# Kernel tuning notes

Hardware: AMD Instinct MI355X
Metric: run time of the kernel (lower is better)

## Reference

```python
import jax, jax.numpy as jnp
import numpy as np

HEADS = 16
DIM = 1024


def setup_inputs() -> dict:
    key = jax.random.key(0)
    ks = jax.random.split(key, 9)
    B, N, D = 2, 2048, DIM
    s = 1.0 / np.sqrt(D)
    x = jax.random.normal(ks[0], (B, N, D), dtype=jnp.float32)
    Wq = jax.random.normal(ks[1], (D, D), dtype=jnp.float32) * s
    Wk = jax.random.normal(ks[2], (D, D), dtype=jnp.float32) * s
    Wv = jax.random.normal(ks[3], (D, D), dtype=jnp.float32) * s
    Wo = jax.random.normal(ks[4], (D, D), dtype=jnp.float32) * s
    bq = jax.random.normal(ks[5], (D,), dtype=jnp.float32) * 0.01
    bk = jax.random.normal(ks[6], (D,), dtype=jnp.float32) * 0.01
    bv = jax.random.normal(ks[7], (D,), dtype=jnp.float32) * 0.01
    bo = jax.random.normal(ks[8], (D,), dtype=jnp.float32) * 0.01
    return {"x": x, "Wq": Wq, "bq": bq, "Wk": Wk, "bk": bk,
            "Wv": Wv, "bv": bv, "Wo": Wo, "bo": bo}


def reference(x, Wq, bq, Wk, bk, Wv, bv, Wo, bo):
    B, N, D = x.shape
    H = HEADS
    hd = D // H
    scale = hd ** (-0.5)
    # projections; split heads -> [B, H, N, hd]
    q = (x @ Wq + bq).reshape(B, N, H, hd).transpose(0, 2, 1, 3)
    k = (x @ Wk + bk).reshape(B, N, H, hd).transpose(0, 2, 1, 3)
    v = (x @ Wv + bv).reshape(B, N, H, hd).transpose(0, 2, 1, 3)
    # full [B, H, N, N] scores (faithful to naive torch implementation)
    attn = jnp.einsum('bhqd,bhkd->bhqk', q, k) * scale
    attn = jax.nn.softmax(attn, axis=-1)
    # dropout is identity in eval mode
    out = jnp.einsum('bhqk,bhkd->bhqd', attn, v)
    out = out.transpose(0, 2, 1, 3).reshape(B, N, D)
    return out @ Wo + bo
```

## Files before the change

kernel.cpp:

```cpp
#include <hip/hip_runtime.h>

#define HEADS 16
#define HD 64
#define SEQ 2048
#define DMODEL 1024
#define BATCH 2
#define MTOT (BATCH*SEQ)
#define KVB 64
#define NKH 16

typedef unsigned short u16;
typedef __bf16 bf16;
typedef bf16 bf16x8 __attribute__((ext_vector_type(8)));
typedef float f32x4 __attribute__((ext_vector_type(4)));
typedef float f32x16 __attribute__((ext_vector_type(16)));
typedef unsigned short u16x8 __attribute__((ext_vector_type(8)));
typedef unsigned short u16x4 __attribute__((ext_vector_type(4)));

static __device__ __forceinline__ u16 f2bf(float f) {
  bf16 b = (bf16)f;
  return __builtin_bit_cast(u16, b);
}

static __device__ __forceinline__ void async16(u16* lds_base, const u16* g) {
  __builtin_amdgcn_global_load_lds(
      (const __attribute__((address_space(1))) unsigned int*)g,
      (__attribute__((address_space(3))) unsigned int*)lds_base,
      16, 0, 0);
}

__global__ __launch_bounds__(256) void k_cvt(const float* __restrict__ in,
                                             u16* __restrict__ out, int n8) {
  int i = blockIdx.x * blockDim.x + threadIdx.x;
  if (i >= n8) return;
  const float4* p = (const float4*)(in + (size_t)i * 8);
  float4 a = p[0], b = p[1];
  u16x8 r;
  r[0] = f2bf(a.x); r[1] = f2bf(a.y); r[2] = f2bf(a.z); r[3] = f2bf(a.w);
  r[4] = f2bf(b.x); r[5] = f2bf(b.y); r[6] = f2bf(b.z); r[7] = f2bf(b.w);
  *(u16x8*)(out + (size_t)i * 8) = r;
}

__global__ __launch_bounds__(256) void k_cvtT(const float* __restrict__ W0, const float* __restrict__ W1,
                                              const float* __restrict__ W2, const float* __restrict__ W3,
                                              u16* __restrict__ T0, u16* __restrict__ T1,
                                              u16* __restrict__ T2, u16* __restrict__ T3) {
  const float* W = blockIdx.z == 0 ? W0 : blockIdx.z == 1 ? W1 : blockIdx.z == 2 ? W2 : W3;
  u16*         T = blockIdx.z == 0 ? T0 : blockIdx.z == 1 ? T1 : blockIdx.z == 2 ? T2 : T3;
  __shared__ u16 tile[64 * 68];
  int t = threadIdx.x;
  int kb = blockIdx.y * 64, nb = blockIdx.x * 64;
#pragma unroll
  for (int i = 0; i < 4; ++i) {
    int c = t * 4 + i;
    int row = c >> 4;
    int c4 = c & 15;
    float4 v = *(const float4*)&W[(size_t)(kb + row) * DMODEL + nb + c4 * 4];
    tile[row * 68 + c4 * 4 + 0] = f2bf(v.x);
    tile[row * 68 + c4 * 4 + 1] = f2bf(v.y);
    tile[row * 68 + c4 * 4 + 2] = f2bf(v.z);
    tile[row * 68 + c4 * 4 + 3] = f2bf(v.w);
  }
  __syncthreads();
#pragma unroll
  for (int i = 0; i < 2; ++i) {
    int c = t * 2 + i;
    int n = c >> 3;
    int k8 = c & 7;
    u16x8 v;
#pragma unroll
    for (int e = 0; e < 8; ++e) v[e] = tile[(k8 * 8 + e) * 68 + n];
    *(u16x8*)&T[(size_t)(nb + n) * DMODEL + kb + k8 * 8] = v;
  }
}

template <int MODE>
__global__ __launch_bounds__(256) void k_gemm(
    const u16* __restrict__ A,
    const u16* __restrict__ BT0, const u16* __restrict__ BT1, const u16* __restrict__ BT2,
    const float* __restrict__ b0, const float* __restrict__ b1, const float* __restrict__ b2,
    void* __restrict__ O0, void* __restrict__ O1, void* __restrict__ O2,
    int M, int N, int K) {
  const u16* BT = blockIdx.z == 0 ? BT0 : blockIdx.z == 1 ? BT1 : BT2;
  const float* bias = blockIdx.z == 0 ? b0 : blockIdx.z == 1 ? b1 : b2;
  void* Out = blockIdx.z == 0 ? O0 : blockIdx.z == 1 ? O1 : O2;

  __shared__ u16 Ads[2][128 * 32];
  __shared__ u16 Bds[2][128 * 32];
  int tid = threadIdx.x, wid = tid >> 6, lane = tid & 63;
  int r = lane & 15, g = lane >> 4;
  int wm = wid >> 1, wn = wid & 1;
  int m0 = blockIdx.y * 128, n0 = blockIdx.x * 128;

  f32x4 acc[4][4];
  f32x4 zero4 = {0.f, 0.f, 0.f, 0.f};
#pragma unroll
  for (int mt = 0; mt < 4; ++mt)
#pragma unroll
    for (int nt = 0; nt < 4; ++nt) acc[mt][nt] = zero4;

  int srow = lane >> 2;
  int scb = lane & 3;

  auto STAGE = [&](int b, int k0) {
#pragma unroll
    for (int tt = 0; tt < 2; ++tt) {
      int inst = wid * 2 + tt;
      int row = inst * 16 + srow;
      async16(&Ads[b][inst * 512], &A[(size_t)(m0 + row) * K + k0 + scb * 8]);
      async16(&Bds[b][inst * 512], &BT[(size_t)(n0 + row) * K + k0 + scb * 8]);
    }
  };

  auto BODY = [&](int buf, int k0) {
    if (k0 + 32 < K) STAGE(buf ^ 1, k0 + 32);
    bf16x8 af[4], bfv[4];
#pragma unroll
    for (int mt = 0; mt < 4; ++mt)
      af[mt] = *(const bf16x8*)&Ads[buf][(wm * 64 + mt * 16 + r) * 32 + g * 8];
#pragma unroll
    for (int nt = 0; nt < 4; ++nt)
      bfv[nt] = *(const bf16x8*)&Bds[buf][(wn * 64 + nt * 16 + r) * 32 + g * 8];
#pragma unroll
    for (int mt = 0; mt < 4; ++mt)
#pragma unroll
      for (int nt = 0; nt < 4; ++nt)
        acc[mt][nt] = __builtin_amdgcn_mfma_f32_16x16x32_bf16(af[mt], bfv[nt], acc[mt][nt], 0, 0, 0);
    asm volatile("s_waitcnt vmcnt(0)" ::: "memory");
    __builtin_amdgcn_sched_barrier(0);
    __builtin_amdgcn_s_barrier();
    __builtin_amdgcn_sched_barrier(0);
  };

  STAGE(0, 0);
  asm volatile("s_waitcnt vmcnt(0)" ::: "memory");
  __builtin_amdgcn_sched_barrier(0);
  __builtin_amdgcn_s_barrier();
  __builtin_amdgcn_sched_barrier(0);

  for (int k0 = 0; k0 < K; k0 += 64) {
    BODY(0, k0);
    BODY(1, k0 + 32);
  }

  const float qs = 0.18033688011112042f;
#pragma unroll
  for (int nt = 0; nt < 4; ++nt) {
    int col = n0 + wn * 64 + nt * 16 + r;
    float bv = bias[col];
#pragma unroll
    for (int mt = 0; mt < 4; ++mt) {
      int rowb = m0 + wm * 64 + mt * 16 + g * 4;
      if (MODE == 0) {
        int b = rowb >> 11;
        int h = col >> 6, d = col & (HD - 1);
        if (blockIdx.z == 2) {
          int n = rowb & (SEQ - 1);
          int np = (n & ~12) | ((n & 4) << 1) | ((n & 8) >> 1);
          u16x4 pk;
#pragma unroll
          for (int j = 0; j < 4; ++j) pk[j] = f2bf(acc[mt][nt][j] + bv);
          *(u16x4*)&((u16*)Out)[((size_t)((b * HEADS + h) * HD + d)) * SEQ + np] = pk;
        } else {
          float sc = (blockIdx.z == 0) ? qs : 1.0f;
#pragma unroll
          for (int j = 0; j < 4; ++j) {
            int row = rowb + j;
            int n = row & (SEQ - 1);
            ((u16*)Out)[((size_t)(b * HEADS + h) * SEQ + n) * HD + d] = f2bf((acc[mt][nt][j] + bv) * sc);
          }
        }
      } else {
#pragma unroll
        for (int j = 0; j < 4; ++j)
          ((float*)Out)[(size_t)(rowb + j) * N + col] = acc[mt][nt][j] + bv;
      }
    }
  }
}

__global__ __launch_bounds__(512, 2) void k_attn(const u16* __restrict__ Q,
                                                 const u16* __restrict__ Kg,
                                                 const u16* __restrict__ Vt,
                                                 u16* __restrict__ Oa) {
  __shared__ u16 lds[2][2][2][KVB * 64];

  int tid = threadIdx.x, wid = tid >> 6, lane = tid & 63;
  int l31 = lane & 31, hi = lane >> 5;
  int h = wid >> 2, s = wid & 3;

  int fid = blockIdx.y * gridDim.x + blockIdx.x;
  int swz = (fid & 7) * 32 + (fid >> 3);
  int qt = swz & 7;
  int bh = swz >> 3;

  const size_t kbase = (size_t)bh * SEQ * HD;
  const size_t vbase = (size_t)bh * HD * SEQ;
  int qA = qt * 256 + s * 64;

  bf16x8 qfA[4], qfB[4];
#pragma unroll
  for (int db = 0; db < 4; ++db) {
    qfA[db] = *(const bf16x8*)&Q[kbase + (size_t)(qA + l31) * HD + db * 16 + hi * 8];
    qfB[db] = *(const bf16x8*)&Q[kbase + (size_t)(qA + 32 + l31) * HD + db * 16 + hi * 8];
  }

  int swz7 = l31 & 7;
  int coff[4];
#pragma unroll
  for (int i = 0; i < 4; ++i) coff[i] = ((2 * i + hi) ^ swz7) * 8;

  f32x16 zero16 = {0.f,0.f,0.f,0.f,0.f,0.f,0.f,0.f,0.f,0.f,0.f,0.f,0.f,0.f,0.f,0.f};
  f32x16 oa0A = zero16, oa1A = zero16, lA = zero16;
  f32x16 oa0B = zero16, oa1B = zero16, lB = zero16;

  u16x8 onesb;
#pragma unroll
  for (int e = 0; e < 8; ++e) onesb[e] = 0x3F80;
  bf16x8 ones = __builtin_bit_cast(bf16x8, onesb);

  auto STAGE = [&](int b, int kc) {
    int kof = (h * NKH + kc) * KVB;
#pragma unroll
    for (int i = 0; i < 2; ++i) {
      int inst = s * 2 + i;
      int rr = inst * 8 + (lane >> 3);
      int ch = (lane & 7) ^ (rr & 7);
      async16(&lds[b][h][0][inst * 512], &Kg[kbase + (size_t)(kof + rr) * HD + ch * 8]);
      async16(&lds[b][h][1][inst * 512], &Vt[vbase + (size_t)rr * SEQ + kof + ch * 8]);
    }
  };

  auto BODY = [&](int buf, int kc) {
    if (kc + 1 < NKH) STAGE(buf ^ 1, kc + 1);

    const u16* Kb = &lds[buf][h][0][0];
    const u16* Vb = &lds[buf][h][1][0];

    f32x16 s0A = zero16, s1A = zero16, s0B = zero16, s1B = zero16;
#pragma unroll
    for (int db = 0; db < 4; ++db) {
      bf16x8 kf0 = *(const bf16x8*)&Kb[l31 * 64 + coff[db]];
      bf16x8 kf1 = *(const bf16x8*)&Kb[2048 + l31 * 64 + coff[db]];
      s0A = __builtin_amdgcn_mfma_f32_32x32x16_bf16(kf0, qfA[db], s0A, 0, 0, 0);
      s1A = __builtin_amdgcn_mfma_f32_32x32x16_bf16(kf1, qfA[db], s1A, 0, 0, 0);
      s0B = __builtin_amdgcn_mfma_f32_32x32x16_bf16(kf0, qfB[db], s0B, 0, 0, 0);
      s1B = __builtin_amdgcn_mfma_f32_32x32x16_bf16(kf1, qfB[db], s1B, 0, 0, 0);
    }

#pragma unroll
    for (int t = 0; t < 4; ++t) {
      u16x8 pkA, pkB;
#pragma unroll
      for (int e = 0; e < 8; ++e) {
        float svA = (t & 2) ? ((t & 1) ? s1A[8 + e] : s1A[e])
                            : ((t & 1) ? s0A[8 + e] : s0A[e]);
        float svB = (t & 2) ? ((t & 1) ? s1B[8 + e] : s1B[e])
                            : ((t & 1) ? s0B[8 + e] : s0B[e]);
        pkA[e] = f2bf(__builtin_amdgcn_exp2f(svA));
        pkB[e] = f2bf(__builtin_amdgcn_exp2f(svB));
      }
      bf16x8 paA = __builtin_bit_cast(bf16x8, pkA);
      bf16x8 paB = __builtin_bit_cast(bf16x8, pkB);

      bf16x8 vf0 = *(const bf16x8*)&Vb[l31 * 64 + coff[t]];
      bf16x8 vf1 = *(const bf16x8*)&Vb[2048 + l31 * 64 + coff[t]];
      lA   = __builtin_amdgcn_mfma_f32_32x32x16_bf16(paA, ones, lA, 0, 0, 0);
      oa0A = __builtin_amdgcn_mfma_f32_32x32x16_bf16(paA, vf0, oa0A, 0, 0, 0);
      oa1A = __builtin_amdgcn_mfma_f32_32x32x16_bf16(paA, vf1, oa1A, 0, 0, 0);
      lB   = __builtin_amdgcn_mfma_f32_32x32x16_bf16(paB, ones, lB, 0, 0, 0);
      oa0B = __builtin_amdgcn_mfma_f32_32x32x16_bf16(paB, vf0, oa0B, 0, 0, 0);
      oa1B = __builtin_amdgcn_mfma_f32_32x32x16_bf16(paB, vf1, oa1B, 0, 0, 0);
    }

    asm volatile("s_waitcnt vmcnt(0)" ::: "memory");
    __builtin_amdgcn_sched_barrier(0);
    __builtin_amdgcn_s_barrier();
    __builtin_amdgcn_sched_barrier(0);
  };

  STAGE(0, 0);
  asm volatile("s_waitcnt vmcnt(0)" ::: "memory");
  __builtin_amdgcn_sched_barrier(0);
  __builtin_amdgcn_s_barrier();
  __builtin_amdgcn_sched_barrier(0);

  for (int kc = 0; kc < NKH; kc += 2) {
    BODY(0, kc);
    BODY(1, kc + 1);
  }

  float* cf = (float*)&lds[0][0][0][0];
  int b = bh >> 4, hh = bh & 15;

  if (h == 1) {
#pragma unroll
    for (int r = 0; r < 16; ++r) {
      cf[s * 3072 + r * 64 + lane]        = oa0A[r];
      cf[s * 3072 + 1024 + r * 64 + lane] = oa1A[r];
      cf[s * 3072 + 2048 + r * 64 + lane] = lA[r];
    }
  }
  __syncthreads();
  if (h == 0) {
#pragma unroll
    for (int reg = 0; reg < 16; ++reg) {
      float o0 = oa0A[reg] + cf[s * 3072 + reg * 64 + lane];
      float o1 = oa1A[reg] + cf[s * 3072 + 1024 + reg * 64 + lane];
      float lv = lA[reg]   + cf[s * 3072 + 2048 + reg * 64 + lane];
      float inv = 1.0f / lv;
      int q = qA + (reg & 3) + 8 * (reg >> 2) + 4 * hi;
      size_t rowoff = ((size_t)(b * SEQ + q)) * DMODEL + hh * HD;
      Oa[rowoff + l31]      = f2bf(o0 * inv);
      Oa[rowoff + 32 + l31] = f2bf(o1 * inv);
    }
  }
  __syncthreads();
  if (h == 1) {
#pragma unroll
    for (int r = 0; r < 16; ++r) {
      cf[s * 3072 + r * 64 + lane]        = oa0B[r];
      cf[s * 3072 + 1024 + r * 64 + lane] = oa1B[r];
      cf[s * 3072 + 2048 + r * 64 + lane] = lB[r];
    }
  }
  __syncthreads();
  if (h == 0) {
#pragma unroll
    for (int reg = 0; reg < 16; ++reg) {
      float o0 = oa0B[reg] + cf[s * 3072 + reg * 64 + lane];
      float o1 = oa1B[reg] + cf[s * 3072 + 1024 + reg * 64 + lane];
      float lv = lB[reg]   + cf[s * 3072 + 2048 + reg * 64 + lane];
      float inv = 1.0f / lv;
      int q = qA + 32 + (reg & 3) + 8 * (reg >> 2) + 4 * hi;
      size_t rowoff = ((size_t)(b * SEQ + q)) * DMODEL + hh * HD;
      Oa[rowoff + l31]      = f2bf(o0 * inv);
      Oa[rowoff + 32 + l31] = f2bf(o1 * inv);
    }
  }
}

extern "C" void kernel_launch(void* const* d_in, const int* in_sizes, int n_in,
                              void* d_out, int out_size, void* d_ws, size_t ws_size,
                              hipStream_t stream) {
  const float* x  = (const float*)d_in[0];
  const float* Wq = (const float*)d_in[1];
  const float* bq = (const float*)d_in[2];
  const float* Wk = (const float*)d_in[3];
  const float* bk = (const float*)d_in[4];
  const float* Wv = (const float*)d_in[5];
  const float* bv = (const float*)d_in[6];
  const float* Wo = (const float*)d_in[7];
  const float* bo = (const float*)d_in[8];

  char* ws = (char*)d_ws;
  const size_t MB = 1024 * 1024;
  u16* xb    = (u16*)(ws);
  u16* wqT   = (u16*)(ws + 8 * MB);
  u16* wkT   = (u16*)(ws + 10 * MB);
  u16* wvT   = (u16*)(ws + 12 * MB);
  u16* woT   = (u16*)(ws + 14 * MB);
  u16* qbuf  = (u16*)(ws + 16 * MB);
  u16* kbuf  = (u16*)(ws + 24 * MB);
  u16* vbufT = (u16*)(ws + 32 * MB);
  u16* abuf  = (u16*)(ws + 40 * MB);

  k_cvt<<<2048, 256, 0, stream>>>(x, xb, (MTOT * DMODEL) / 8);
  k_cvtT<<<dim3(16, 16, 4), 256, 0, stream>>>(Wq, Wk, Wv, Wo, wqT, wkT, wvT, woT);
  k_gemm<0><<<dim3(DMODEL / 128, MTOT / 128, 3), 256, 0, stream>>>(
      xb, wqT, wkT, wvT, bq, bk, bv, qbuf, kbuf, vbufT, MTOT, DMODEL, DMODEL);
  k_attn<<<dim3(SEQ / 256, BATCH * HEADS), 512, 0, stream>>>(qbuf, kbuf, vbufT, abuf);
  k_gemm<1><<<dim3(DMODEL / 128, MTOT / 128, 1), 256, 0, stream>>>(
      abuf, woT, woT, woT, bo, bo, bo, d_out, d_out, d_out, MTOT, DMODEL, DMODEL);
}
```

Baseline: 111.2 us.

## Split-K output projection GEMM across two wave groups with LDS reduction

Replaces the templated output-projection GEMM with a dedicated 512-thread kernel. Two halves of the block each process half of K for the same 128x128 tile, and their partial accumulators are reduced through LDS before the bias is added and the result written. The output projection launches only 256 tiles of 256 threads, so this is meant to put more waves on each CU and hide latency, with a swizzled tile order for cache locality. The cost is an extra LDS reduction, a sync, and higher register and LDS pressure.

```diff
diff --git a/kernel.cpp b/kernel.cpp
--- a/kernel.cpp
+++ b/kernel.cpp
@@ -74,7 +74,6 @@
   }
 }
 
-template <int MODE>
 __global__ __launch_bounds__(256) void k_gemm(
     const u16* __restrict__ A,
     const u16* __restrict__ BT0, const u16* __restrict__ BT1, const u16* __restrict__ BT2,
@@ -151,29 +150,126 @@
 #pragma unroll
     for (int mt = 0; mt < 4; ++mt) {
       int rowb = m0 + wm * 64 + mt * 16 + g * 4;
-      if (MODE == 0) {
-        int b = rowb >> 11;
-        int h = col >> 6, d = col & (HD - 1);
-        if (blockIdx.z == 2) {
-          int n = rowb & (SEQ - 1);
-          int np = (n & ~12) | ((n & 4) << 1) | ((n & 8) >> 1);
-          u16x4 pk;
-#pragma unroll
-          for (int j = 0; j < 4; ++j) pk[j] = f2bf(acc[mt][nt][j] + bv);
-          *(u16x4*)&((u16*)Out)[((size_t)((b * HEADS + h) * HD + d)) * SEQ + np] = pk;
-        } else {
-          float sc = (blockIdx.z == 0) ? qs : 1.0f;
-#pragma unroll
-          for (int j = 0; j < 4; ++j) {
-            int row = rowb + j;
-            int n = row & (SEQ - 1);
-            ((u16*)Out)[((size_t)(b * HEADS + h) * SEQ + n) * HD + d] = f2bf((acc[mt][nt][j] + bv) * sc);
-          }
+      int b = rowb >> 11;
+      int h = col >> 6, d = col & (HD - 1);
+      if (blockIdx.z == 2) {
+        int n = rowb & (SEQ - 1);
+        int np = (n & ~12) | ((n & 4) << 1) | ((n & 8) >> 1);
+        u16x4 pk;
+#pragma unroll
+        for (int j = 0; j < 4; ++j) pk[j] = f2bf(acc[mt][nt][j] + bv);
+        *(u16x4*)&((u16*)Out)[((size_t)((b * HEADS + h) * HD + d)) * SEQ + np] = pk;
+      } else {
+        float sc = (blockIdx.z == 0) ? qs : 1.0f;
+#pragma unroll
+        for (int j = 0; j < 4; ++j) {
+          int row = rowb + j;
+          int n = row & (SEQ - 1);
+          ((u16*)Out)[((size_t)(b * HEADS + h) * SEQ + n) * HD + d] = f2bf((acc[mt][nt][j] + bv) * sc);
         }
-      } else {
+      }
+    }
+  }
+}
+
+__global__ __launch_bounds__(512, 2) void k_gemm1(
+    const u16* __restrict__ A, const u16* __restrict__ BT,
+    const float* __restrict__ bias, float* __restrict__ Out,
+    int M, int N, int K) {
+  __shared__ u16 smem[32768];
+  u16* Apart = smem;
+  u16* Bpart = smem + 16384;
+
+  int tid = threadIdx.x, wid = tid >> 6, lane = tid & 63;
+  int r = lane & 15, g = lane >> 4;
+  int h = wid >> 2, w = wid & 3;
+  int wm = w >> 1, wn = w & 1;
+
+  int fid = blockIdx.y * gridDim.x + blockIdx.x;
+  int nb = (fid & 7) * 32 + (fid >> 3);
+  int m0 = (nb >> 3) * 128, n0 = (nb & 7) * 128;
+
+  f32x4 acc[4][4];
+  f32x4 zero4 = {0.f, 0.f, 0.f, 0.f};
+#pragma unroll
+  for (int mt = 0; mt < 4; ++mt)
+#pragma unroll
+    for (int nt = 0; nt < 4; ++nt) acc[mt][nt] = zero4;
+
+  int srow = lane >> 2;
+  int scb = lane & 3;
+  const int KH = K >> 1;
+
+  auto STAGE = [&](int b, int k0) {
+    int kg = h * KH + k0;
+#pragma unroll
+    for (int tt = 0; tt < 2; ++tt) {
+      int inst = w * 2 + tt;
+      int row = inst * 16 + srow;
+      async16(&Apart[((b * 2 + h) * 8 + inst) * 512], &A[(size_t)(m0 + row) * K + kg + scb * 8]);
+      async16(&Bpart[((b * 2 + h) * 8 + inst) * 512], &BT[(size_t)(n0 + row) * K + kg + scb * 8]);
+    }
+  };
+
+  auto BODY = [&](int buf, int k0) {
+    if (k0 + 32 < KH) STAGE(buf ^ 1, k0 + 32);
+    const u16* Ab = &Apart[(buf * 2 + h) * 4096];
+    const u16* Bb = &Bpart[(buf * 2 + h) * 4096];
+    bf16x8 af[4], bfv[4];
+#pragma unroll
+    for (int mt = 0; mt < 4; ++mt)
+      af[mt] = *(const bf16x8*)&Ab[(wm * 64 + mt * 16 + r) * 32 + g * 8];
+#pragma unroll
+    for (int nt = 0; nt < 4; ++nt)
+      bfv[nt] = *(const bf16x8*)&Bb[(wn * 64 + nt * 16 + r) * 32 + g * 8];
+#pragma unroll
+    for (int mt = 0; mt < 4; ++mt)
+#pragma unroll
+      for (int nt = 0; nt < 4; ++nt)
+        acc[mt][nt] = __builtin_amdgcn_mfma_f32_16x16x32_bf16(af[mt], bfv[nt], acc[mt][nt], 0, 0, 0);
+    asm volatile("s_waitcnt vmcnt(0)" ::: "memory");
+    __builtin_amdgcn_sched_barrier(0);
+    __builtin_amdgcn_s_barrier();
+    __builtin_amdgcn_sched_barrier(0);
+  };
+
+  STAGE(0, 0);
+  asm volatile("s_waitcnt vmcnt(0)" ::: "memory");
+  __builtin_amdgcn_sched_barrier(0);
+  __builtin_amdgcn_s_barrier();
+  __builtin_amdgcn_sched_barrier(0);
+
+  for (int k0 = 0; k0 < KH; k0 += 64) {
+    BODY(0, k0);
+    BODY(1, k0 + 32);
+  }
+
+  __syncthreads();
+  float* cfp = (float*)smem;
+  if (h == 1) {
+#pragma unroll
+    for (int mt = 0; mt < 4; ++mt)
+#pragma unroll
+      for (int nt = 0; nt < 4; ++nt)
 #pragma unroll
         for (int j = 0; j < 4; ++j)
-          ((float*)Out)[(size_t)(rowb + j) * N + col] = acc[mt][nt][j] + bv;
+          cfp[(wm * 64 + mt * 16 + g * 4 + j) * 128 + wn * 64 + nt * 16 + r] = acc[mt][nt][j];
+  }
+  __syncthreads();
+  if (h == 0) {
+#pragma unroll
+    for (int nt = 0; nt < 4; ++nt) {
+      int col = n0 + wn * 64 + nt * 16 + r;
+      float bv = bias[col];
+#pragma unroll
+      for (int mt = 0; mt < 4; ++mt) {
+        int rowb = m0 + wm * 64 + mt * 16 + g * 4;
+#pragma unroll
+        for (int j = 0; j < 4; ++j) {
+          float v = acc[mt][nt][j] + bv +
+                    cfp[(wm * 64 + mt * 16 + g * 4 + j) * 128 + wn * 64 + nt * 16 + r];
+          Out[(size_t)(rowb + j) * N + col] = v;
+        }
       }
     }
   }
@@ -295,10 +391,10 @@
 
   if (h == 1) {
 #pragma unroll
-    for (int r = 0; r < 16; ++r) {
-      cf[s * 3072 + r * 64 + lane]        = oa0A[r];
-      cf[s * 3072 + 1024 + r * 64 + lane] = oa1A[r];
-      cf[s * 3072 + 2048 + r * 64 + lane] = lA[r];
+    for (int r2 = 0; r2 < 16; ++r2) {
+      cf[s * 3072 + r2 * 64 + lane]        = oa0A[r2];
+      cf[s * 3072 + 1024 + r2 * 64 + lane] = oa1A[r2];
+      cf[s * 3072 + 2048 + r2 * 64 + lane] = lA[r2];
     }
   }
   __syncthreads();
@@ -318,10 +414,10 @@
   __syncthreads();
   if (h == 1) {
 #pragma unroll
-    for (int r = 0; r < 16; ++r) {
-      cf[s * 3072 + r * 64 + lane]        = oa0B[r];
-      cf[s * 3072 + 1024 + r * 64 + lane] = oa1B[r];
-      cf[s * 3072 + 2048 + r * 64 + lane] = lB[r];
+    for (int r2 = 0; r2 < 16; ++r2) {
+      cf[s * 3072 + r2 * 64 + lane]        = oa0B[r2];
+      cf[s * 3072 + 1024 + r2 * 64 + lane] = oa1B[r2];
+      cf[s * 3072 + 2048 + r2 * 64 + lane] = lB[r2];
     }
   }
   __syncthreads();
@@ -367,9 +463,9 @@
 
   k_cvt<<<2048, 256, 0, stream>>>(x, xb, (MTOT * DMODEL) / 8);
   k_cvtT<<<dim3(16, 16, 4), 256, 0, stream>>>(Wq, Wk, Wv, Wo, wqT, wkT, wvT, woT);
-  k_gemm<0><<<dim3(DMODEL / 128, MTOT / 128, 3), 256, 0, stream>>>(
+  k_gemm<<<dim3(DMODEL / 128, MTOT / 128, 3), 256, 0, stream>>>(
       xb, wqT, wkT, wvT, bq, bk, bv, qbuf, kbuf, vbufT, MTOT, DMODEL, DMODEL);
   k_attn<<<dim3(SEQ / 256, BATCH * HEADS), 512, 0, stream>>>(qbuf, kbuf, vbufT, abuf);
-  k_gemm<1><<<dim3(DMODEL / 128, MTOT / 128, 1), 256, 0, stream>>>(
-      abuf, woT, woT, woT, bo, bo, bo, d_out, d_out, d_out, MTOT, DMODEL, DMODEL);
-}
+  k_gemm1<<<dim3(DMODEL / 128, MTOT / 128), 512, 0, stream>>>(
+      abuf, woT, bo, (float*)d_out, MTOT, DMODEL, DMODEL);
+}
```

After: 105.9 us. 1.05x faster.
